# Kernel tuning notes

Measured on AMD Instinct MI355X. Metric: run time of the kernel, lower is better.

Reference implementation:

```python
import jax, jax.numpy as jnp
import numpy as np

E, M, B, S = 1024, 256, 4, 2048
LN_EPS = 1e-5

def _l2norm(x):
    # F.normalize(p=2, dim=-1, eps=1e-12)
    n = jnp.linalg.norm(x, axis=-1, keepdims=True)
    return x / jnp.maximum(n, 1e-12)

def _layernorm(x, g, b):
    mu = jnp.mean(x, axis=-1, keepdims=True)
    var = jnp.var(x, axis=-1, keepdims=True)
    return (x - mu) * jax.lax.rsqrt(var + LN_EPS) * g + b

def setup_inputs() -> dict:
    key = jax.random.key(0)
    ks = jax.random.split(key, 16)
    s = 0.02
    inp = {
        'x': jax.random.normal(ks[0], (B, S, E), jnp.float32),
        'memory': jnp.zeros((B, M, M), jnp.float32),
        'w_k': jax.random.normal(ks[1], (M, E), jnp.float32) * s,
        'b_k': jnp.zeros((M,), jnp.float32),
        'w_q': jax.random.normal(ks[2], (M, E), jnp.float32) * s,
        'b_q': jnp.zeros((M,), jnp.float32),
        'w_v': jax.random.normal(ks[3], (M, E), jnp.float32) * s,
        'b_v': jnp.zeros((M,), jnp.float32),
        'w_out': jax.random.normal(ks[4], (E, M), jnp.float32) * s,
        'b_out': jnp.zeros((E,), jnp.float32),
        'w_gw': jax.random.normal(ks[5], (1, E), jnp.float32) * s,
        'b_gw': jnp.full((1,), -2.0, jnp.float32),
        'w_gf': jax.random.normal(ks[6], (1, E), jnp.float32) * s,
        'b_gf': jnp.full((1,), 2.0, jnp.float32),
        'ln1_g': jnp.ones((E,), jnp.float32),
        'ln1_b': jnp.zeros((E,), jnp.float32),
        'ln2_g': jnp.ones((E,), jnp.float32),
        'ln2_b': jnp.zeros((E,), jnp.float32),
        'w_f1': jax.random.normal(ks[7], (4 * E, E), jnp.float32) * s,
        'b_f1': jnp.zeros((4 * E,), jnp.float32),
        'w_f2': jax.random.normal(ks[8], (E, 4 * E), jnp.float32) * s,
        'b_f2': jnp.zeros((E,), jnp.float32),
    }
    return inp

def reference(x, memory, w_k, b_k, w_q, b_q, w_v, b_v, w_out, b_out,
              w_gw, b_gw, w_gf, b_gf, ln1_g, ln1_b, ln2_g, ln2_b,
              w_f1, b_f1, w_f2, b_f2):
    xn = _layernorm(x, ln1_g, ln1_b)                      # [B,S,E]
    k_all = _l2norm(xn @ w_k.T + b_k)                     # [B,S,M]
    q_all = _l2norm(xn @ w_q.T + b_q)                     # [B,S,M]
    v_all = jnp.tanh(xn @ w_v.T + b_v)                    # [B,S,M]
    beta_all = jax.nn.sigmoid(xn @ w_gw.T + b_gw)         # [B,S,1]
    decay_all = jax.nn.sigmoid(xn @ w_gf.T + b_gf)        # [B,S,1]

    def step(mem, inps):
        k, q, v, beta, decay = inps                       # k,q,v:[B,M]; beta,decay:[B,1]
        readout = jnp.einsum('bij,bj->bi', mem, q)        # read BEFORE update
        assoc = v[:, :, None] * k[:, None, :]             # [B,M,M] outer product
        mem = decay[:, :, None] * mem + beta[:, :, None] * assoc
        return mem, readout

    seq = (jnp.swapaxes(k_all, 0, 1), jnp.swapaxes(q_all, 0, 1),
           jnp.swapaxes(v_all, 0, 1), jnp.swapaxes(beta_all, 0, 1),
           jnp.swapaxes(decay_all, 0, 1))
    new_memory, readouts = jax.lax.scan(step, memory, seq)  # readouts: [S,B,M]
    stacked = jnp.swapaxes(readouts, 0, 1)                  # [B,S,M]
    mixer_out = stacked @ w_out.T + b_out                   # [B,S,E]

    x = x + mixer_out
    h = _layernorm(x, ln2_g, ln2_b)
    ffn = jax.nn.gelu(h @ w_f1.T + b_f1, approximate=False) @ w_f2.T + b_f2
    x = x + ffn
    return (x, new_memory)
```

## Files before the change

kernel.cpp:

```cpp
#include <hip/hip_runtime.h>
#include <stdint.h>

#define E_DIM 1024
#define M_DIM 256
#define B_DIM 4
#define S_DIM 2048
#define NTOK  8192
#define CHUNK 64
#define NCHUNK 32
#define NCB   128

typedef unsigned short u16;
typedef unsigned int   u32;
typedef __attribute__((ext_vector_type(8))) short short8;
typedef __attribute__((ext_vector_type(4))) float floatx4;

#define OFF_WKQV   ((size_t)0)
#define OFF_WOUT   ((size_t)1572864)
#define OFF_WF1    ((size_t)2097152)
#define OFF_WF2    ((size_t)10485760)
#define OFF_BKQV   ((size_t)18874368)
#define OFF_BETA   ((size_t)18877440)
#define OFF_DECAY  ((size_t)18910208)
#define OFF_P      ((size_t)18942976)
#define OFF_WW     ((size_t)18976256)
#define OFF_ABUF   ((size_t)19009024)
#define OFF_XN     ((size_t)21106176)
#define OFF_KQV    ((size_t)37883392)
#define OFF_T      ((size_t)63049216)
#define OFF_STATES ((size_t)96603648)
#define OFF_RO     ((size_t)130158080)
#define OFF_H      OFF_XN
#define OFF_Y1     OFF_T
#define OFF_G      OFF_STATES
#define OFF_P2     OFF_XN

__device__ __forceinline__ u16 f2bf(float f) {
    union { float f; u32 u; } a; a.f = f;
    u32 u = a.u;
    return (u16)((u + 0x7fffu + ((u >> 16) & 1u)) >> 16);
}
__device__ __forceinline__ u32 pack2bf(float a, float b) {
    return (u32)f2bf(a) | ((u32)f2bf(b) << 16);
}
__device__ __forceinline__ float sigmoidf_(float x) { return 1.0f / (1.0f + expf(-x)); }

__device__ __forceinline__ void gload_lds16(const u16* g, u16* l) {
    __builtin_amdgcn_global_load_lds((const __attribute__((address_space(1))) void*)g,
                                     (__attribute__((address_space(3))) void*)l, 16, 0, 0);
}

__device__ __forceinline__ int sw_slot(int idx) {
    return ((idx & 3) ^ ((idx >> 3) & 3)) * 8;
}
__device__ __forceinline__ int sw_read(int row, int kc) {
    return row * 32 + ((kc ^ ((row >> 1) & 3)) << 3);
}

__device__ __forceinline__ void block_reduce_2(float& a, float& b, float* red, int t) {
#pragma unroll
    for (int o = 32; o > 0; o >>= 1) { a += __shfl_xor(a, o); b += __shfl_xor(b, o); }
    if ((t & 63) == 0) { red[t >> 6] = a; red[4 + (t >> 6)] = b; }
    __syncthreads();
    a = red[0] + red[1] + red[2] + red[3];
    b = red[4] + red[5] + red[6] + red[7];
    __syncthreads();
}

__device__ __forceinline__ uint2 cvt4(float4 v) {
    uint2 o; o.x = pack2bf(v.x, v.y); o.y = pack2bf(v.z, v.w); return o;
}
__global__ void convert_weights(const float4* __restrict__ wk, const float4* __restrict__ wq,
                                const float4* __restrict__ wv, const float4* __restrict__ wo,
                                const float4* __restrict__ wf1in, const float4* __restrict__ wf2in,
                                const float* __restrict__ bk, const float* __restrict__ bq,
                                const float* __restrict__ bv,
                                uint2* __restrict__ wkqv, uint2* __restrict__ wout,
                                uint2* __restrict__ wf1, uint2* __restrict__ wf2,
                                float* __restrict__ bkqv) {
    int b = blockIdx.x, t = threadIdx.x;
    if (b < 768) {
        int i = b * 256 + t;
        int sec = i >> 16, off = i & 65535;
        const float4* s = (sec == 0) ? wk : ((sec == 1) ? wq : wv);
        wkqv[i] = cvt4(s[off]);
    } else if (b < 1024) {
        int i = (b - 768) * 256 + t;
        wout[i] = cvt4(wo[i]);
    } else if (b < 5120) {
        int i = (b - 1024) * 256 + t;
        wf1[i] = cvt4(wf1in[i]);
    } else if (b < 9216) {
        int i = (b - 5120) * 256 + t;
        wf2[i] = cvt4(wf2in[i]);
    } else {
        bkqv[t] = bk[t]; bkqv[256 + t] = bq[t]; bkqv[512 + t] = bv[t];
    }
}

__global__ __launch_bounds__(256) void ln1_gates(
    const float* __restrict__ x, const float* __restrict__ g, const float* __restrict__ b,
    const float* __restrict__ wgw, const float* __restrict__ bgw,
    const float* __restrict__ wgf, const float* __restrict__ bgf,
    u16* __restrict__ xn, float* __restrict__ beta, float* __restrict__ decay)
{
    __shared__ float red[8];
    const int row = blockIdx.x;
    const int t = threadIdx.x;
    const float4 v = ((const float4*)(x + (size_t)row * E_DIM))[t];
    float s  = v.x + v.y + v.z + v.w;
    float ss = v.x * v.x + v.y * v.y + v.z * v.z + v.w * v.w;
    block_reduce_2(s, ss, red, t);
    const float mean = s * (1.0f / E_DIM);
    const float var  = ss * (1.0f / E_DIM) - mean * mean;
    const float rstd = rsqrtf(var + 1e-5f);
    const float4 gg = ((const float4*)g)[t];
    const float4 bb = ((const float4*)b)[t];
    float4 xnv;
    xnv.x = (v.x - mean) * rstd * gg.x + bb.x;
    xnv.y = (v.y - mean) * rstd * gg.y + bb.y;
    xnv.z = (v.z - mean) * rstd * gg.z + bb.z;
    xnv.w = (v.w - mean) * rstd * gg.w + bb.w;
    uint2 o; o.x = pack2bf(xnv.x, xnv.y); o.y = pack2bf(xnv.z, xnv.w);
    ((uint2*)(xn + (size_t)row * E_DIM))[t] = o;
    const float4 w1 = ((const float4*)wgw)[t];
    const float4 w2 = ((const float4*)wgf)[t];
    float dg = xnv.x * w1.x + xnv.y * w1.y + xnv.z * w1.z + xnv.w * w1.w;
    float df = xnv.x * w2.x + xnv.y * w2.y + xnv.z * w2.z + xnv.w * w2.w;
    block_reduce_2(dg, df, red, t);
    if (t == 0) {
        beta[row]  = sigmoidf_(dg + bgw[0]);
        decay[row] = sigmoidf_(df + bgf[0]);
    }
}

__global__ __launch_bounds__(256) void ln2_kernel(
    const float* __restrict__ y1, const float* __restrict__ g, const float* __restrict__ b,
    u16* __restrict__ h)
{
    __shared__ float red[8];
    const int row = blockIdx.x;
    const int t = threadIdx.x;
    const float4 v = ((const float4*)(y1 + (size_t)row * E_DIM))[t];
    float s  = v.x + v.y + v.z + v.w;
    float ss = v.x * v.x + v.y * v.y + v.z * v.z + v.w * v.w;
    block_reduce_2(s, ss, red, t);
    const float mean = s * (1.0f / E_DIM);
    const float var  = ss * (1.0f / E_DIM) - mean * mean;
    const float rstd = rsqrtf(var + 1e-5f);
    const float4 gg = ((const float4*)g)[t];
    const float4 bb = ((const float4*)b)[t];
    float4 xnv;
    xnv.x = (v.x - mean) * rstd * gg.x + bb.x;
    xnv.y = (v.y - mean) * rstd * gg.y + bb.y;
    xnv.z = (v.z - mean) * rstd * gg.z + bb.z;
    xnv.w = (v.w - mean) * rstd * gg.w + bb.w;
    uint2 o; o.x = pack2bf(xnv.x, xnv.y); o.y = pack2bf(xnv.z, xnv.w);
    ((uint2*)(h + (size_t)row * E_DIM))[t] = o;
}

__global__ __launch_bounds__(256) void kqv_act(float* __restrict__ pA,
                                               const float* __restrict__ pB,
                                               const float* __restrict__ bias) {
    __shared__ float red[8];
    const int row = blockIdx.x;
    const int t = threadIdx.x;
    float* p = pA + (size_t)row * 768;
    const float* q = pB + (size_t)row * 768;
    float kv = p[t]       + q[t]       + bias[t];
    float qv = p[256 + t] + q[256 + t] + bias[256 + t];
    float vv = p[512 + t] + q[512 + t] + bias[512 + t];
    float sk = kv * kv, sq = qv * qv;
    block_reduce_2(sk, sq, red, t);
    float nk = fmaxf(sqrtf(sk), 1e-12f);
    float nq = fmaxf(sqrtf(sq), 1e-12f);
    p[t]       = kv / nk;
    p[256 + t] = qv / nq;
    p[512 + t] = tanhf(vv);
}

__global__ void chunk_prep(const float* __restrict__ beta, const float* __restrict__ decay,
                           float* __restrict__ P, float* __restrict__ ww) {
    int cb = blockIdx.x;
    int b = cb >> 5, c = cb & 31;
    int tb = b * S_DIM + c * CHUNK;
    int j = threadIdx.x;
    __shared__ float d[64], bt[64], Ps[65];
    d[j]  = decay[tb + j];
    bt[j] = beta[tb + j];
    __syncthreads();
    if (j == 0) {
        float p = 1.0f; Ps[0] = 1.0f;
        for (int i = 0; i < 64; i++) { p *= d[i]; Ps[i + 1] = p; }
    }
    __syncthreads();
    P[cb * 65 + j] = Ps[j];
    if (j == 0) P[cb * 65 + 64] = Ps[64];
    ww[cb * 64 + j] = bt[j] / Ps[j + 1];
}

__global__ __launch_bounds__(256) void t_kernel(const float* __restrict__ kqv,
                                                const float* __restrict__ P,
                                                const float* __restrict__ ww,
                                                float* __restrict__ T) {
    int cb = blockIdx.y;
    int tile = blockIdx.x;
    int r0 = (tile >> 2) * 64, c0 = (tile & 3) * 64;
    int b = cb >> 5, c = cb & 31;
    int tb = b * S_DIM + c * CHUNK;
    float p64 = P[cb * 65 + 64];
    __shared__ float Vs[64][65], Ks[64][65];
    int t = threadIdx.x;
#pragma unroll
    for (int i = 0; i < 16; i++) {
        int idx = t + i * 256; int j = idx >> 6, col = idx & 63;
        float sc = ww[cb * 64 + j] * p64;
        Vs[j][col] = kqv[(size_t)(tb + j) * 768 + 512 + r0 + col] * sc;
        Ks[j][col] = kqv[(size_t)(tb + j) * 768 + 0   + c0 + col];
    }
    __syncthreads();
    int tr = t >> 4, tc = t & 15;
    float a[4][4] = {};
    for (int j = 0; j < 64; j++) {
        float vv[4], kk[4];
#pragma unroll
        for (int r = 0; r < 4; r++)  vv[r] = Vs[j][tr * 4 + r];
#pragma unroll
        for (int cc = 0; cc < 4; cc++) kk[cc] = Ks[j][tc * 4 + cc];
#pragma unroll
        for (int r = 0; r < 4; r++)
#pragma unroll
            for (int cc = 0; cc < 4; cc++) a[r][cc] += vv[r] * kk[cc];
    }
#pragma unroll
    for (int r = 0; r < 4; r++)
#pragma unroll
        for (int cc = 0; cc < 4; cc++)
            T[(size_t)cb * 65536 + (size_t)(r0 + tr * 4 + r) * 256 + (c0 + tc * 4 + cc)] = a[r][cc];
}

__global__ void mem_scan(const float* __restrict__ mem0, const float* __restrict__ T,
                         const float* __restrict__ P, float* __restrict__ states,
                         float* __restrict__ memOut) {
    int gid = blockIdx.x * 256 + threadIdx.x;
    int b = gid >> 16; int e = gid & 65535;
    float s = mem0[gid];
    for (int c = 0; c < NCHUNK; c++) {
        int cb = b * NCHUNK + c;
        states[(size_t)cb * 65536 + e] = s;
        s = P[cb * 65 + 64] * s + T[(size_t)cb * 65536 + e];
    }
    memOut[gid] = s;
}

__global__ __launch_bounds__(256) void qk_attn(const float* __restrict__ kqv,
                                               const float* __restrict__ P,
                                               const float* __restrict__ ww,
                                               float* __restrict__ Abuf) {
    int cb = blockIdx.x;
    int b = cb >> 5, c = cb & 31;
    int tb = b * S_DIM + c * CHUNK;
    __shared__ float Qs[64][65], Ks[64][65];
    int t = threadIdx.x;
    int tr = t >> 4, tc = t & 15;
    float acc[4][4] = {};
    for (int kt = 0; kt < 4; kt++) {
        __syncthreads();
#pragma unroll
        for (int i = 0; i < 16; i++) {
            int idx = t + i * 256; int rr = idx >> 6, cc2 = idx & 63;
            Qs[rr][cc2] = kqv[(size_t)(tb + rr) * 768 + 256 + kt * 64 + cc2];
            Ks[rr][cc2] = kqv[(size_t)(tb + rr) * 768 + 0   + kt * 64 + cc2];
        }
        __syncthreads();
        for (int kk = 0; kk < 64; kk++) {
            float qq[4], kx[4];
#pragma unroll
            for (int r = 0; r < 4; r++)  qq[r] = Qs[tr * 4 + r][kk];
#pragma unroll
            for (int cc = 0; cc < 4; cc++) kx[cc] = Ks[tc * 4 + cc][kk];
#pragma unroll
            for (int r = 0; r < 4; r++)
#pragma unroll
                for (int cc = 0; cc < 4; cc++) acc[r][cc] += qq[r] * kx[cc];
        }
    }
#pragma unroll
    for (int r = 0; r < 4; r++) {
#pragma unroll
        for (int cc = 0; cc < 4; cc++) {
            int i = tr * 4 + r, j = tc * 4 + cc;
            float v = (j < i) ? acc[r][cc] * (P[cb * 65 + i] * ww[cb * 64 + j]) : 0.0f;
            Abuf[(size_t)cb * 4096 + i * 64 + j] = v;
        }
    }
}

__global__ __launch_bounds__(256) void readout_k(const float* __restrict__ kqv,
                                                 const float* __restrict__ Abuf,
                                                 const float* __restrict__ states,
                                                 const float* __restrict__ P,
                                                 u16* __restrict__ ro) {
    int cb = blockIdx.y;
    int rt = blockIdx.x;
    int b = cb >> 5, c = cb & 31;
    int tb = b * S_DIM + c * CHUNK;
    int r0 = rt * 64;
    __shared__ float As[64][65], Vs[64][65], Qs[64][65], Ms[64][65];
    int t = threadIdx.x;
    int tr = t >> 4, tc = t & 15;
#pragma unroll
    for (int i = 0; i < 16; i++) {
        int idx = t + i * 256; int rr = idx >> 6, cc2 = idx & 63;
        As[rr][cc2] = Abuf[(size_t)cb * 4096 + rr * 64 + cc2];
        Vs[rr][cc2] = kqv[(size_t)(tb + rr) * 768 + 512 + r0 + cc2];
    }
    __syncthreads();
    float acc[4][4] = {};
    for (int j = 0; j < 64; j++) {
        float aa[4], vv[4];
#pragma unroll
        for (int r = 0; r < 4; r++)  aa[r] = As[tr * 4 + r][j];
#pragma unroll
        for (int cc = 0; cc < 4; cc++) vv[cc] = Vs[j][tc * 4 + cc];
#pragma unroll
        for (int r = 0; r < 4; r++)
#pragma unroll
            for (int cc = 0; cc < 4; cc++) acc[r][cc] += aa[r] * vv[cc];
    }
    float acc2[4][4] = {};
    for (int kt = 0; kt < 4; kt++) {
        __syncthreads();
#pragma unroll
        for (int i = 0; i < 16; i++) {
            int idx = t + i * 256; int rr = idx >> 6, cc2 = idx & 63;
            Qs[rr][cc2] = kqv[(size_t)(tb + rr) * 768 + 256 + kt * 64 + cc2];
            Ms[rr][cc2] = states[(size_t)cb * 65536 + (size_t)(r0 + rr) * 256 + kt * 64 + cc2];
        }
        __syncthreads();
        for (int kk = 0; kk < 64; kk++) {
            float qq[4], mm[4];
#pragma unroll
            for (int r = 0; r < 4; r++)  qq[r] = Qs[tr * 4 + r][kk];
#pragma unroll
            for (int cc = 0; cc < 4; cc++) mm[cc] = Ms[tc * 4 + cc][kk];
#pragma unroll
            for (int r = 0; r < 4; r++)
#pragma unroll
                for (int cc = 0; cc < 4; cc++) acc2[r][cc] += qq[r] * mm[cc];
        }
    }
#pragma unroll
    for (int r = 0; r < 4; r++) {
#pragma unroll
        for (int cc = 0; cc < 4; cc++) {
            int i = tr * 4 + r;
            float val = acc[r][cc] + P[cb * 65 + i] * acc2[r][cc];
            ro[(size_t)(tb + i) * 256 + r0 + tc * 4 + cc] = f2bf(val);
        }
    }
}

__global__ __launch_bounds__(256) void combine_k(float4* __restrict__ out,
                                                 const float4* __restrict__ part) {
    int i = blockIdx.x * 256 + threadIdx.x;
    float4 a = out[i], b = part[i];
    a.x += b.x; a.y += b.y; a.z += b.z; a.w += b.w;
    out[i] = a;
}

#define EPI_BIAS   0
#define EPI_RESID  1
#define EPI_GELU   2
#define EPI_SPART  3
#define EPI_SRESID 4

template<int EPI, int BM, int MY, int SQH, int SQW>
__global__ __launch_bounds__(256) void gemm_bt(
    const u16* __restrict__ A, int lda,
    const u16* __restrict__ B, int ldb,
    const float* __restrict__ bias,
    const float* __restrict__ resid,
    float* __restrict__ outF, u16* __restrict__ outB,
    int ldc, int K, float* __restrict__ part)
{
    constexpr int MI = BM / 32;
    __shared__ u16 As[3][BM * 32];
    __shared__ u16 Bs[3][128 * 32];
    const int t = threadIdx.x;
    const int lane = t & 63;
    const int w = t >> 6;
    const int waveM = (w >> 1) * (BM / 2);
    const int waveN = (w & 1) * 64;

    int bx, by;
    if (MY == 0) {
        bx = blockIdx.x; by = blockIdx.y;
    } else {
        const u32 NX = gridDim.x;
        u32 flat = blockIdx.x + NX * blockIdx.y;
        u32 xcd = flat & 7;
        u32 local = flat >> 3;
        u32 perBand = (u32)SQH * NX;
        u32 band = local / perBand;
        u32 rem  = local - band * perBand;
        u32 sq   = rem / (SQH * SQW);
        u32 wloc = rem - sq * (SQH * SQW);
        u32 wy = wloc / SQW, wx = wloc - wy * SQW;
        by = xcd * MY + band * SQH + wy;
        bx = sq * SQW + wx;
    }

    const int m0 = by * BM;
    const int n0 = bx * 128;
    const size_t koff = (size_t)blockIdx.z * K;

    const int sr = t >> 2, scw = sw_slot(t);
    const u16* Ag0 = A + (size_t)(m0 + sr) * lda + koff + scw;
    const u16* Ag1 = A + (size_t)(m0 + 64 + sr) * lda + koff + scw;
    const u16* Bg0 = B + (size_t)(n0 + sr) * ldb + koff + scw;
    const u16* Bg1 = B + (size_t)(n0 + 64 + sr) * ldb + koff + scw;

    floatx4 acc[MI][4] = {};

    const int kc = lane >> 4;
    const int rsel = lane & 15;
    const int NK = K >> 5;

    gload_lds16(Ag0, As[0] + t * 8);
    if (BM == 128) gload_lds16(Ag1, As[0] + (t + 256) * 8);
    gload_lds16(Bg0, Bs[0] + t * 8);
    gload_lds16(Bg1, Bs[0] + (t + 256) * 8);
    gload_lds16(Ag0 + 32, As[1] + t * 8);
    if (BM == 128) gload_lds16(Ag1 + 32, As[1] + (t + 256) * 8);
    gload_lds16(Bg0 + 32, Bs[1] + t * 8);
    gload_lds16(Bg1 + 32, Bs[1] + (t + 256) * 8);
    if constexpr (BM == 128) { asm volatile("s_waitcnt vmcnt(4)" ::: "memory"); }
    else                     { asm volatile("s_waitcnt vmcnt(3)" ::: "memory"); }
    __builtin_amdgcn_s_barrier();
    __builtin_amdgcn_sched_barrier(0);

    int cur = 0, nx1 = 1, nx2 = 2;
    for (int kt = 0; kt < NK; kt++) {
        if (kt + 2 < NK) {
            const int kof = (kt + 2) * 32;
            u16* Ad = As[nx2];
            u16* Bd = Bs[nx2];
            gload_lds16(Ag0 + kof, Ad + t * 8);
            if (BM == 128) gload_lds16(Ag1 + kof, Ad + (t + 256) * 8);
            gload_lds16(Bg0 + kof, Bd + t * 8);
            gload_lds16(Bg1 + kof, Bd + (t + 256) * 8);
        }
        const u16* Ac = As[cur];
        const u16* Bc = Bs[cur];
        short8 af[MI], bfr[4];
#pragma unroll
        for (int i = 0; i < MI; i++)
            af[i] = *(const short8*)(Ac + sw_read(waveM + i * 16 + rsel, kc));
#pragma unroll
        for (int j = 0; j < 4; j++)
            bfr[j] = *(const short8*)(Bs[cur] + sw_read(waveN + j * 16 + rsel, kc));
#pragma unroll
        for (int i = 0; i < MI; i++)
#pragma unroll
            for (int j = 0; j < 4; j++)
                acc[i][j] = __builtin_amdgcn_mfma_f32_16x16x32_bf16(af[i], bfr[j], acc[i][j], 0, 0, 0);
        if (kt + 2 < NK) {
            if constexpr (BM == 128) { asm volatile("s_waitcnt vmcnt(4)" ::: "memory"); }
            else                     { asm volatile("s_waitcnt vmcnt(3)" ::: "memory"); }
        } else {
            asm volatile("s_waitcnt vmcnt(0)" ::: "memory");
        }
        __builtin_amdgcn_s_barrier();
        __builtin_amdgcn_sched_barrier(0);
        const int tmp = cur; cur = nx1; nx1 = nx2; nx2 = tmp;
    }

    const bool zmain = (blockIdx.z == 0);
    const int rbase = (lane >> 4) * 4;
#pragma unroll
    for (int i = 0; i < MI; i++) {
#pragma unroll
        for (int j = 0; j < 4; j++) {
            const int col = n0 + waveN + j * 16 + rsel;
            float bv = 0.0f;
            if (EPI == EPI_BIAS || EPI == EPI_RESID || EPI == EPI_GELU) bv = bias[col];
            if (EPI == EPI_SRESID && zmain) bv = bias[col];
#pragma unroll
            for (int r = 0; r < 4; r++) {
                const int row = m0 + waveM + i * 16 + rbase + r;
                const size_t oidx = (size_t)row * ldc + col;
                float v = acc[i][j][r] + bv;
                if (EPI == EPI_BIAS) {
                    outF[oidx] = v;
                } else if (EPI == EPI_RESID) {
                    outF[oidx] = v + resid[oidx];
                } else if (EPI == EPI_GELU) {
                    float gl = 0.5f * v * (1.0f + erff(v * 0.70710678118654752f));
                    outB[oidx] = f2bf(gl);
                } else if (EPI == EPI_SPART) {
                    (zmain ? outF : part)[oidx] = v;
                } else {
                    if (zmain) outF[oidx] = v + resid[oidx];
                    else       part[oidx] = v;
                }
            }
        }
    }
}

__device__ __forceinline__ void g8_stage(const u16* As, const u16* Bs, int lda, int ldb,
                                         u16* la, u16* lb, int t, int ko) {
    gload_lds16(As + ko, la + t * 8);
    gload_lds16(As + (size_t)128 * lda + ko, la + 4096 + t * 8);
    gload_lds16(Bs + ko, lb + t * 8);
    gload_lds16(Bs + (size_t)128 * ldb + ko, lb + 4096 + t * 8);
}
__device__ __forceinline__ void g8_frags(const u16* LA, const u16* LB,
                                         int wm, int wn, int rsel, int kc,
                                         short8 (&af)[8], short8 (&bv)[4]) {
#pragma unroll
    for (int i = 0; i < 8; i++)
        af[i] = *(const short8*)(LA + sw_read(wm * 128 + i * 16 + rsel, kc));
#pragma unroll
    for (int j = 0; j < 4; j++)
        bv[j] = *(const short8*)(LB + sw_read(wn * 64 + j * 16 + rsel, kc));
}
__device__ __forceinline__ void g8_mfma(short8 (&af)[8], short8 (&bv)[4], floatx4 (&acc)[8][4]) {
    __builtin_amdgcn_s_setprio(1);
#pragma unroll
    for (int i = 0; i < 8; i++)
#pragma unroll
        for (int j = 0; j < 4; j++)
            acc[i][j] = __builtin_amdgcn_mfma_f32_16x16x32_bf16(af[i], bv[j], acc[i][j], 0, 0, 0);
    __builtin_amdgcn_s_setprio(0);
}

template<int EPI, int MY, int SQH, int SQW>
__global__ __launch_bounds__(512, 2) void gemm8(
    const u16* __restrict__ A, int lda,
    const u16* __restrict__ B, int ldb,
    const float* __restrict__ bias,
    const float* __restrict__ resid,
    float* __restrict__ outF, u16* __restrict__ outB,
    int ldc, int K, float* __restrict__ part)
{
    __shared__ u16 L[2][2][2][8192];
    const int t = threadIdx.x;
    const int lane = t & 63;
    const int w = t >> 6;
    const int wm = w >> 2;
    const int wn = w & 3;
    const int kc = lane >> 4;
    const int rsel = lane & 15;

    int bx, by;
    {
        const u32 NX = gridDim.x;
        u32 flat = blockIdx.x + NX * blockIdx.y;
        u32 xcd = flat & 7;
        u32 local = flat >> 3;
        u32 perBand = (u32)SQH * NX;
        u32 band = local / perBand;
        u32 rem  = local - band * perBand;
        u32 sq   = rem / (SQH * SQW);
        u32 wloc = rem - sq * (SQH * SQW);
        u32 wy = wloc / SQW, wx = wloc - wy * SQW;
        by = xcd * MY + band * SQH + wy;
        bx = sq * SQW + wx;
    }
    const int m0 = by * 256;
    const int n0 = bx * 256;
    const size_t koff = (size_t)blockIdx.z * K;

    const int srow = t >> 2;
    const int scw  = sw_slot(t);
    const u16* Asrc = A + (size_t)(m0 + srow) * lda + koff + scw;
    const u16* Bsrc = B + (size_t)(n0 + srow) * ldb + koff + scw;

    floatx4 acc[8][4] = {};
    const int NT = K >> 6;

    g8_stage(Asrc, Bsrc, lda, ldb, &L[0][0][0][0], &L[0][1][0][0], t, 0);
    g8_stage(Asrc, Bsrc, lda, ldb, &L[0][0][1][0], &L[0][1][1][0], t, 32);
    if (NT > 1)
        g8_stage(Asrc, Bsrc, lda, ldb, &L[1][0][0][0], &L[1][1][0][0], t, 64);

    for (int tt = 0; tt + 1 < NT; ++tt) {
        const int cb = tt & 1;
        asm volatile("s_waitcnt vmcnt(8)" ::: "memory");
        __builtin_amdgcn_s_barrier();
        __builtin_amdgcn_sched_barrier(0);
        {
            short8 af[8], bv[4];
            g8_frags(&L[cb][0][0][0], &L[cb][1][0][0], wm, wn, rsel, kc, af, bv);
            g8_stage(Asrc, Bsrc, lda, ldb, &L[cb ^ 1][0][1][0], &L[cb ^ 1][1][1][0], t,
                     (tt + 1) * 64 + 32);
            asm volatile("s_waitcnt lgkmcnt(0)" ::: "memory");
            __builtin_amdgcn_sched_barrier(0);
            g8_mfma(af, bv, acc);
        }
        asm volatile("s_waitcnt vmcnt(8)" ::: "memory");
        __builtin_amdgcn_s_barrier();
        __builtin_amdgcn_sched_barrier(0);
        {
            short8 af[8], bv[4];
            g8_frags(&L[cb][0][1][0], &L[cb][1][1][0], wm, wn, rsel, kc, af, bv);
            if (tt + 2 < NT)
                g8_stage(Asrc, Bsrc, lda, ldb, &L[cb][0][0][0], &L[cb][1][0][0], t,
                         (tt + 2) * 64);
            asm volatile("s_waitcnt lgkmcnt(0)" ::: "memory");
            __builtin_amdgcn_sched_barrier(0);
            g8_mfma(af, bv, acc);
        }
    }
    {
        const int cb = (NT - 1) & 1;
        asm volatile("s_waitcnt vmcnt(4)" ::: "memory");
        __builtin_amdgcn_s_barrier();
        __builtin_amdgcn_sched_barrier(0);
        {
            short8 af[8], bv[4];
            g8_frags(&L[cb][0][0][0], &L[cb][1][0][0], wm, wn, rsel, kc, af, bv);
            asm volatile("s_waitcnt lgkmcnt(0)" ::: "memory");
            __builtin_amdgcn_sched_barrier(0);
            g8_mfma(af, bv, acc);
        }
        asm volatile("s_waitcnt vmcnt(0)" ::: "memory");
        __builtin_amdgcn_s_barrier();
        __builtin_amdgcn_sched_barrier(0);
        {
            short8 af[8], bv[4];
            g8_frags(&L[cb][0][1][0], &L[cb][1][1][0], wm, wn, rsel, kc, af, bv);
            asm volatile("s_waitcnt lgkmcnt(0)" ::: "memory");
            __builtin_amdgcn_sched_barrier(0);
            g8_mfma(af, bv, acc);
        }
    }

    const bool zmain = (blockIdx.z == 0);
    const int rbase = kc * 4;
#pragma unroll
    for (int i = 0; i < 8; i++) {
#pragma unroll
        for (int j = 0; j < 4; j++) {
            const int col = n0 + wn * 64 + j * 16 + rsel;
            float bv = 0.0f;
            if (EPI == EPI_BIAS || EPI == EPI_RESID || EPI == EPI_GELU) bv = bias[col];
            if (EPI == EPI_SRESID && zmain) bv = bias[col];
#pragma unroll
            for (int r = 0; r < 4; r++) {
                const int row = m0 + wm * 128 + i * 16 + rbase + r;
                const size_t oidx = (size_t)row * ldc + col;
                float v = acc[i][j][r] + bv;
                if (EPI == EPI_BIAS) {
                    outF[oidx] = v;
                } else if (EPI == EPI_RESID) {
                    outF[oidx] = v + resid[oidx];
                } else if (EPI == EPI_GELU) {
                    float gl = 0.5f * v * (1.0f + erff(v * 0.70710678118654752f));
                    outB[oidx] = f2bf(gl);
                } else if (EPI == EPI_SPART) {
                    (zmain ? outF : part)[oidx] = v;
                } else {
                    if (zmain) outF[oidx] = v + resid[oidx];
                    else       part[oidx] = v;
                }
            }
        }
    }
}

extern "C" void kernel_launch(void* const* d_in, const int* in_sizes, int n_in,
                              void* d_out, int out_size, void* d_ws, size_t ws_size,
                              hipStream_t stream) {
    const float* x     = (const float*)d_in[0];
    const float* mem0  = (const float*)d_in[1];
    const float* w_k   = (const float*)d_in[2];
    const float* b_k   = (const float*)d_in[3];
    const float* w_q   = (const float*)d_in[4];
    const float* b_q   = (const float*)d_in[5];
    const float* w_v   = (const float*)d_in[6];
    const float* b_v   = (const float*)d_in[7];
    const float* w_out = (const float*)d_in[8];
    const float* b_out = (const float*)d_in[9];
    const float* w_gw  = (const float*)d_in[10];
    const float* b_gw  = (const float*)d_in[11];
    const float* w_gf  = (const float*)d_in[12];
    const float* b_gf  = (const float*)d_in[13];
    const float* ln1g  = (const float*)d_in[14];
    const float* ln1b  = (const float*)d_in[15];
    const float* ln2g  = (const float*)d_in[16];
    const float* ln2b  = (const float*)d_in[17];
    const float* w_f1  = (const float*)d_in[18];
    const float* b_f1  = (const float*)d_in[19];
    const float* w_f2  = (const float*)d_in[20];
    const float* b_f2  = (const float*)d_in[21];

    char* ws = (char*)d_ws;
    u16*   wkqv  = (u16*)(ws + OFF_WKQV);
    u16*   wout  = (u16*)(ws + OFF_WOUT);
    u16*   wf1   = (u16*)(ws + OFF_WF1);
    u16*   wf2   = (u16*)(ws + OFF_WF2);
    float* bkqv  = (float*)(ws + OFF_BKQV);
    float* beta  = (float*)(ws + OFF_BETA);
    float* decay = (float*)(ws + OFF_DECAY);
    float* P     = (float*)(ws + OFF_P);
    float* ww    = (float*)(ws + OFF_WW);
    float* Abuf  = (float*)(ws + OFF_ABUF);
    u16*   xn    = (u16*)(ws + OFF_XN);
    float* kqv   = (float*)(ws + OFF_KQV);
    float* kqvPB = (float*)(ws + OFF_T);
    float* T     = (float*)(ws + OFF_T);
    float* states= (float*)(ws + OFF_STATES);
    u16*   ro    = (u16*)(ws + OFF_RO);
    u16*   h     = (u16*)(ws + OFF_H);
    float* y1    = (float*)(ws + OFF_Y1);
    u16*   g     = (u16*)(ws + OFF_G);
    float* p2    = (float*)(ws + OFF_P2);

    float* out_x   = (float*)d_out;
    float* out_mem = out_x + (size_t)NTOK * E_DIM;

    convert_weights<<<9217, 256, 0, stream>>>(
        (const float4*)w_k, (const float4*)w_q, (const float4*)w_v,
        (const float4*)w_out, (const float4*)w_f1, (const float4*)w_f2,
        b_k, b_q, b_v,
        (uint2*)wkqv, (uint2*)wout, (uint2*)wf1, (uint2*)wf2, bkqv);

    ln1_gates<<<NTOK, 256, 0, stream>>>(x, ln1g, ln1b, w_gw, b_gw, w_gf, b_gf, xn, beta, decay);

    gemm_bt<EPI_SPART, 128, 0, 0, 0><<<dim3(6, 64, 2), 256, 0, stream>>>(
        xn, 1024, wkqv, 1024, nullptr, nullptr, kqv, nullptr, 768, 512, kqvPB);
    kqv_act<<<NTOK, 256, 0, stream>>>(kqv, kqvPB, bkqv);

    chunk_prep<<<NCB, 64, 0, stream>>>(beta, decay, P, ww);
    t_kernel<<<dim3(16, NCB), 256, 0, stream>>>(kqv, P, ww, T);
    mem_scan<<<1024, 256, 0, stream>>>(mem0, T, P, states, out_mem);
    qk_attn<<<NCB, 256, 0, stream>>>(kqv, P, ww, Abuf);
    readout_k<<<dim3(4, NCB), 256, 0, stream>>>(kqv, Abuf, states, P, ro);

    gemm_bt<EPI_RESID, 64, 0, 0, 0><<<dim3(8, 128), 256, 0, stream>>>(
        ro, 256, wout, 256, b_out, x, y1, nullptr, 1024, 256, nullptr);

    ln2_kernel<<<NTOK, 256, 0, stream>>>(y1, ln2g, ln2b, h);
    gemm8<EPI_GELU, 4, 4, 4><<<dim3(16, 32), 512, 0, stream>>>(
        h, 1024, wf1, 1024, b_f1, nullptr, nullptr, g, 4096, 1024, nullptr);
    gemm8<EPI_SRESID, 4, 4, 4><<<dim3(4, 32, 2), 512, 0, stream>>>(
        g, 4096, wf2, 4096, b_f2, y1, out_x, nullptr, 1024, 2048, p2);
    combine_k<<<8192, 256, 0, stream>>>((float4*)out_x, (const float4*)p2);
}
```

Baseline: 524.0 us.

## Rework GEMM pipelines: four-slot ring in gemm8, double buffer in gemm_bt

The large gemm8 kernel swaps its two-phase double-buffered 64-wide K schedule for a four-slot ring of 32-wide K stages. Each stage is prefetched three steps ahead, and each step needs one barrier plus one vmcnt wait. The aim is fewer barriers and deeper load lookahead within the same LDS footprint. The smaller gemm_bt kernel drops from a triple-buffered explicit-waitcnt scheme to a plain double buffer synchronised with __syncthreads. That frees LDS but exposes more global-load latency.

```diff
diff --git a/kernel.cpp b/kernel.cpp
--- a/kernel.cpp
+++ b/kernel.cpp
@@ -385,8 +385,8 @@
     int ldc, int K, float* __restrict__ part)
 {
     constexpr int MI = BM / 32;
-    __shared__ u16 As[3][BM * 32];
-    __shared__ u16 Bs[3][128 * 32];
+    __shared__ u16 As[2][BM * 32];
+    __shared__ u16 Bs[2][128 * 32];
     const int t = threadIdx.x;
     const int lane = t & 63;
     const int w = t >> 6;
@@ -431,32 +431,21 @@
     if (BM == 128) gload_lds16(Ag1, As[0] + (t + 256) * 8);
     gload_lds16(Bg0, Bs[0] + t * 8);
     gload_lds16(Bg1, Bs[0] + (t + 256) * 8);
-    gload_lds16(Ag0 + 32, As[1] + t * 8);
-    if (BM == 128) gload_lds16(Ag1 + 32, As[1] + (t + 256) * 8);
-    gload_lds16(Bg0 + 32, Bs[1] + t * 8);
-    gload_lds16(Bg1 + 32, Bs[1] + (t + 256) * 8);
-    if constexpr (BM == 128) { asm volatile("s_waitcnt vmcnt(4)" ::: "memory"); }
-    else                     { asm volatile("s_waitcnt vmcnt(3)" ::: "memory"); }
-    __builtin_amdgcn_s_barrier();
-    __builtin_amdgcn_sched_barrier(0);
-
-    int cur = 0, nx1 = 1, nx2 = 2;
+
     for (int kt = 0; kt < NK; kt++) {
-        if (kt + 2 < NK) {
-            const int kof = (kt + 2) * 32;
-            u16* Ad = As[nx2];
-            u16* Bd = Bs[nx2];
-            gload_lds16(Ag0 + kof, Ad + t * 8);
-            if (BM == 128) gload_lds16(Ag1 + kof, Ad + (t + 256) * 8);
-            gload_lds16(Bg0 + kof, Bd + t * 8);
-            gload_lds16(Bg1 + kof, Bd + (t + 256) * 8);
-        }
-        const u16* Ac = As[cur];
-        const u16* Bc = Bs[cur];
+        __syncthreads();
+        const int cur = kt & 1;
+        if (kt + 1 < NK) {
+            const int kof = (kt + 1) * 32;
+            gload_lds16(Ag0 + kof, As[cur ^ 1] + t * 8);
+            if (BM == 128) gload_lds16(Ag1 + kof, As[cur ^ 1] + (t + 256) * 8);
+            gload_lds16(Bg0 + kof, Bs[cur ^ 1] + t * 8);
+            gload_lds16(Bg1 + kof, Bs[cur ^ 1] + (t + 256) * 8);
+        }
         short8 af[MI], bfr[4];
 #pragma unroll
         for (int i = 0; i < MI; i++)
-            af[i] = *(const short8*)(Ac + sw_read(waveM + i * 16 + rsel, kc));
+            af[i] = *(const short8*)(As[cur] + sw_read(waveM + i * 16 + rsel, kc));
 #pragma unroll
         for (int j = 0; j < 4; j++)
             bfr[j] = *(const short8*)(Bs[cur] + sw_read(waveN + j * 16 + rsel, kc));
@@ -465,15 +454,6 @@
 #pragma unroll
             for (int j = 0; j < 4; j++)
                 acc[i][j] = __builtin_amdgcn_mfma_f32_16x16x32_bf16(af[i], bfr[j], acc[i][j], 0, 0, 0);
-        if (kt + 2 < NK) {
-            if constexpr (BM == 128) { asm volatile("s_waitcnt vmcnt(4)" ::: "memory"); }
-            else                     { asm volatile("s_waitcnt vmcnt(3)" ::: "memory"); }
-        } else {
-            asm volatile("s_waitcnt vmcnt(0)" ::: "memory");
-        }
-        __builtin_amdgcn_s_barrier();
-        __builtin_amdgcn_sched_barrier(0);
-        const int tmp = cur; cur = nx1; nx1 = nx2; nx2 = tmp;
     }
 
     const bool zmain = (blockIdx.z == 0);
@@ -509,13 +489,6 @@
     }
 }
 
-__device__ __forceinline__ void g8_stage(const u16* As, const u16* Bs, int lda, int ldb,
-                                         u16* la, u16* lb, int t, int ko) {
-    gload_lds16(As + ko, la + t * 8);
-    gload_lds16(As + (size_t)128 * lda + ko, la + 4096 + t * 8);
-    gload_lds16(Bs + ko, lb + t * 8);
-    gload_lds16(Bs + (size_t)128 * ldb + ko, lb + 4096 + t * 8);
-}
 __device__ __forceinline__ void g8_frags(const u16* LA, const u16* LB,
                                          int wm, int wn, int rsel, int kc,
                                          short8 (&af)[8], short8 (&bv)[4]) {
@@ -545,7 +518,7 @@
     float* __restrict__ outF, u16* __restrict__ outB,
     int ldc, int K, float* __restrict__ part)
 {
-    __shared__ u16 L[2][2][2][8192];
+    __shared__ u16 L[4][2][8192];
     const int t = threadIdx.x;
     const int lane = t & 63;
     const int w = t >> 6;
@@ -579,63 +552,36 @@
     const u16* Bsrc = B + (size_t)(n0 + srow) * ldb + koff + scw;
 
     floatx4 acc[8][4] = {};
-    const int NT = K >> 6;
-
-    g8_stage(Asrc, Bsrc, lda, ldb, &L[0][0][0][0], &L[0][1][0][0], t, 0);
-    g8_stage(Asrc, Bsrc, lda, ldb, &L[0][0][1][0], &L[0][1][1][0], t, 32);
-    if (NT > 1)
-        g8_stage(Asrc, Bsrc, lda, ldb, &L[1][0][0][0], &L[1][1][0][0], t, 64);
-
-    for (int tt = 0; tt + 1 < NT; ++tt) {
-        const int cb = tt & 1;
-        asm volatile("s_waitcnt vmcnt(8)" ::: "memory");
+    const int NR = (K >> 5);
+
+    auto STAGE = [&](int r) {
+        const int ko = r * 32;
+        u16* la = &L[r & 3][0][0];
+        u16* lb = &L[r & 3][1][0];
+        gload_lds16(Asrc + ko, la + t * 8);
+        gload_lds16(Asrc + (size_t)128 * lda + ko, la + 4096 + t * 8);
+        gload_lds16(Bsrc + ko, lb + t * 8);
+        gload_lds16(Bsrc + (size_t)128 * ldb + ko, lb + 4096 + t * 8);
+    };
+
+    STAGE(0); STAGE(1); STAGE(2);
+    asm volatile("s_waitcnt vmcnt(8)" ::: "memory");
+    __builtin_amdgcn_s_barrier();
+    __builtin_amdgcn_sched_barrier(0);
+
+    for (int p = 0; p < NR; ++p) {
+        short8 af[8], bv[4];
+        g8_frags(&L[p & 3][0][0], &L[p & 3][1][0], wm, wn, rsel, kc, af, bv);
+        if (p + 1 < NR) {
+            if (p + 2 < NR) { asm volatile("s_waitcnt vmcnt(4)" ::: "memory"); }
+            else            { asm volatile("s_waitcnt vmcnt(0)" ::: "memory"); }
+        }
         __builtin_amdgcn_s_barrier();
         __builtin_amdgcn_sched_barrier(0);
-        {
-            short8 af[8], bv[4];
-            g8_frags(&L[cb][0][0][0], &L[cb][1][0][0], wm, wn, rsel, kc, af, bv);
-            g8_stage(Asrc, Bsrc, lda, ldb, &L[cb ^ 1][0][1][0], &L[cb ^ 1][1][1][0], t,
-                     (tt + 1) * 64 + 32);
-            asm volatile("s_waitcnt lgkmcnt(0)" ::: "memory");
-            __builtin_amdgcn_sched_barrier(0);
-            g8_mfma(af, bv, acc);
-        }
-        asm volatile("s_waitcnt vmcnt(8)" ::: "memory");
-        __builtin_amdgcn_s_barrier();
+        if (p + 3 < NR) STAGE(p + 3);
+        asm volatile("s_waitcnt lgkmcnt(0)" ::: "memory");
         __builtin_amdgcn_sched_barrier(0);
-        {
-            short8 af[8], bv[4];
-            g8_frags(&L[cb][0][1][0], &L[cb][1][1][0], wm, wn, rsel, kc, af, bv);
-            if (tt + 2 < NT)
-                g8_stage(Asrc, Bsrc, lda, ldb, &L[cb][0][0][0], &L[cb][1][0][0], t,
-                         (tt + 2) * 64);
-            asm volatile("s_waitcnt lgkmcnt(0)" ::: "memory");
-            __builtin_amdgcn_sched_barrier(0);
-            g8_mfma(af, bv, acc);
-        }
-    }
-    {
-        const int cb = (NT - 1) & 1;
-        asm volatile("s_waitcnt vmcnt(4)" ::: "memory");
-        __builtin_amdgcn_s_barrier();
-        __builtin_amdgcn_sched_barrier(0);
-        {
-            short8 af[8], bv[4];
-            g8_frags(&L[cb][0][0][0], &L[cb][1][0][0], wm, wn, rsel, kc, af, bv);
-            asm volatile("s_waitcnt lgkmcnt(0)" ::: "memory");
-            __builtin_amdgcn_sched_barrier(0);
-            g8_mfma(af, bv, acc);
-        }
-        asm volatile("s_waitcnt vmcnt(0)" ::: "memory");
-        __builtin_amdgcn_s_barrier();
-        __builtin_amdgcn_sched_barrier(0);
-        {
-            short8 af[8], bv[4];
-            g8_frags(&L[cb][0][1][0], &L[cb][1][1][0], wm, wn, rsel, kc, af, bv);
-            asm volatile("s_waitcnt lgkmcnt(0)" ::: "memory");
-            __builtin_amdgcn_sched_barrier(0);
-            g8_mfma(af, bv, acc);
-        }
+        g8_mfma(af, bv, acc);
     }
 
     const bool zmain = (blockIdx.z == 0);
@@ -645,14 +591,14 @@
 #pragma unroll
         for (int j = 0; j < 4; j++) {
             const int col = n0 + wn * 64 + j * 16 + rsel;
-            float bv = 0.0f;
-            if (EPI == EPI_BIAS || EPI == EPI_RESID || EPI == EPI_GELU) bv = bias[col];
-            if (EPI == EPI_SRESID && zmain) bv = bias[col];
+            float bvv = 0.0f;
+            if (EPI == EPI_BIAS || EPI == EPI_RESID || EPI == EPI_GELU) bvv = bias[col];
+            if (EPI == EPI_SRESID && zmain) bvv = bias[col];
 #pragma unroll
             for (int r = 0; r < 4; r++) {
                 const int row = m0 + wm * 128 + i * 16 + rbase + r;
                 const size_t oidx = (size_t)row * ldc + col;
-                float v = acc[i][j][r] + bv;
+                float v = acc[i][j][r] + bvv;
                 if (EPI == EPI_BIAS) {
                     outF[oidx] = v;
                 } else if (EPI == EPI_RESID) {
```

After: 520.9 us. About the same (-0.6%).
